# Performance work log

Measured on AMD Instinct MI355X. Metric: run time of the kernel, lower is better.

## Reference

```python
import jax, jax.numpy as jnp
import numpy as np

N = 8192
H_CHANNELS = 2048
HEADS = 16
D = H_CHANNELS // HEADS  # 128


def setup_inputs() -> dict:
    key = jax.random.key(0)
    k1, k2, k3 = jax.random.split(key, 3)
    x0 = jax.random.normal(k1, (N, H_CHANNELS), dtype=jnp.float32)
    # boolean mask: True entries are masked out (set to -inf)
    mask = jax.random.randint(k2, (N, N), 0, 2).astype(jnp.bool_)
    # torch Linear weight layout: [out_features, in_features] = [3*d, h_channels]
    W_qkv = jax.random.normal(k3, (3 * D, H_CHANNELS), dtype=jnp.float32) * (1.0 / np.sqrt(H_CHANNELS))
    return {"x0": x0, "mask": mask, "W_qkv": W_qkv}


def reference(x0, mask, W_qkv):
    # qkv = x0 @ W^T : [N, 3d]
    qkv = x0 @ W_qkv.T
    q, k, v = jnp.split(qkv, 3, axis=-1)          # each [N, d]
    att_logits = (q @ k.T) / D                    # [N, N]  (note: scale is /d, not /sqrt(d))
    att_logits = jnp.where(mask, -jnp.inf, att_logits)
    att = jax.nn.softmax(att_logits, axis=-1)     # [N, N]
    # dropout p=0.0 (eval mode) -> identity
    return att @ v                                # [N, d]
```

## Files before the change

kernel.cpp:

```cpp
#include <hip/hip_runtime.h>
#include <hip/hip_bf16.h>

typedef __attribute__((ext_vector_type(8))) short short8;
typedef __attribute__((ext_vector_type(4))) float f32x4;
typedef __attribute__((ext_vector_type(16))) float f32x16;
typedef __attribute__((ext_vector_type(2))) unsigned int uint2v;

#define NTOK 8192
#define HCH  2048
#define DDIM 128
#define NSPLIT 8
#define KPS   (NTOK / NSPLIT)
#define NITER (KPS / 64)

__device__ __forceinline__ unsigned short f2bf(float f) {
    __hip_bfloat16 h = __float2bfloat16(f);
    return *reinterpret_cast<unsigned short*>(&h);
}
__device__ __forceinline__ unsigned short f2h(float f) {
    _Float16 h = (_Float16)f;
    return *reinterpret_cast<unsigned short*>(&h);
}

__device__ __forceinline__ void gload_lds16(const void* g, void* l) {
    __builtin_amdgcn_global_load_lds(
        reinterpret_cast<const __attribute__((address_space(1))) unsigned int*>(
            reinterpret_cast<uintptr_t>(g)),
        reinterpret_cast<__attribute__((address_space(3))) unsigned int*>(
            reinterpret_cast<uintptr_t>(l)),
        16, 0, 0);
}

__global__ void detect_kernel(const unsigned int* __restrict__ X,
                              const unsigned int* __restrict__ M,
                              int* __restrict__ flags)
{
    const int lane = threadIdx.x & 63;
    unsigned int e = (X[lane] >> 7) & 0xFF;
    unsigned long long hb = __ballot(e >= 110 && e <= 140);

    bool w_ok = true, h_ok = true, b_ok = true;
#pragma unroll
    for (int i = 0; i < 16; i++) {
        unsigned int u = M[lane + 64 * i];
        if (!(u == 0u || u == 1u || u == 0x3F800000u)) w_ok = false;
        unsigned int h0 = u & 0xFFFFu, h1 = u >> 16;
        bool o0 = (h0 == 0u || h0 == 0x3F80u || h0 == 0x3C00u || h0 == 1u);
        bool o1 = (h1 == 0u || h1 == 0x3F80u || h1 == 0x3C00u || h1 == 1u);
        if (!(o0 && o1)) h_ok = false;
        unsigned int b0 = u & 0xFF, b1 = (u >> 8) & 0xFF,
                     b2 = (u >> 16) & 0xFF, b3 = u >> 24;
        if (b0 > 1u || b1 > 1u || b2 > 1u || b3 > 1u) b_ok = false;
    }
    bool allw = __all(w_ok), allh = __all(h_ok), allb = __all(b_ok);
    if (lane == 0) {
        flags[0] = (__popcll(hb) < 32) ? 1 : 0;
        flags[1] = allw ? 0 : (allb ? 1 : (allh ? 2 : 3));
    }
}

__global__ __launch_bounds__(256) void conv_w(
    const void* __restrict__ Wv, const int* __restrict__ flags,
    unsigned short* __restrict__ Wbf)
{
    int t = blockIdx.x * 256 + threadIdx.x;
    size_t off = (size_t)t * 8;
    if (flags[0] != 0) {
        const float* Wf = (const float*)Wv;
        float4 a = *reinterpret_cast<const float4*>(Wf + off);
        float4 b = *reinterpret_cast<const float4*>(Wf + off + 4);
        unsigned short o[8] = { f2bf(a.x), f2bf(a.y), f2bf(a.z), f2bf(a.w),
                                f2bf(b.x), f2bf(b.y), f2bf(b.z), f2bf(b.w) };
        *reinterpret_cast<uint4*>(Wbf + off) = *reinterpret_cast<uint4*>(o);
    } else {
        *reinterpret_cast<uint4*>(Wbf + off) =
            *reinterpret_cast<const uint4*>((const unsigned short*)Wv + off);
    }
}

__global__ __launch_bounds__(256) void conv_x(
    const void* __restrict__ Xv, const int* __restrict__ flags,
    unsigned short* __restrict__ Xbf)
{
    int t = blockIdx.x * 256 + threadIdx.x;
    size_t off = (size_t)t * 8;
    if (flags[0] != 0) {
        const float* Xf = (const float*)Xv;
        float4 a = *reinterpret_cast<const float4*>(Xf + off);
        float4 b = *reinterpret_cast<const float4*>(Xf + off + 4);
        unsigned short o[8] = { f2bf(a.x), f2bf(a.y), f2bf(a.z), f2bf(a.w),
                                f2bf(b.x), f2bf(b.y), f2bf(b.z), f2bf(b.w) };
        *reinterpret_cast<uint4*>(Xbf + off) = *reinterpret_cast<uint4*>(o);
    } else {
        *reinterpret_cast<uint4*>(Xbf + off) =
            *reinterpret_cast<const uint4*>((const unsigned short*)Xv + off);
    }
}

__global__ __launch_bounds__(256) void mask_pack(
    const void* __restrict__ maskv, const int* __restrict__ flags,
    unsigned char* __restrict__ Mp)
{
    const int mmode = flags[1];
    const int NB = NTOK * (NTOK / 8);
    int t0 = blockIdx.x * 256 + threadIdx.x;
    for (int b = t0; b < NB; b += 2048 * 256) {
        unsigned int byte = 0;
        if (mmode == 0) {
            const uint4* p = reinterpret_cast<const uint4*>(
                (const unsigned int*)maskv + (size_t)b * 8);
            uint4 a = p[0], c = p[1];
            byte = (a.x != 0u) | ((a.y != 0u) << 1) | ((a.z != 0u) << 2) | ((a.w != 0u) << 3)
                 | ((c.x != 0u) << 4) | ((c.y != 0u) << 5) | ((c.z != 0u) << 6) | ((c.w != 0u) << 7);
        } else if (mmode == 1) {
            unsigned long long v = *reinterpret_cast<const unsigned long long*>(
                (const unsigned char*)maskv + (size_t)b * 8);
#pragma unroll
            for (int k = 0; k < 8; k++)
                byte |= (((v >> (8 * k)) & 0xFFull) != 0ull) << k;
        } else if (mmode == 2) {
            uint4 a = *reinterpret_cast<const uint4*>(
                (const unsigned short*)maskv + (size_t)b * 8);
            byte = ((a.x & 0xFFFFu) != 0u) | ((a.x >> 16 != 0u) << 1)
                 | (((a.y & 0xFFFFu) != 0u) << 2) | ((a.y >> 16 != 0u) << 3)
                 | (((a.z & 0xFFFFu) != 0u) << 4) | ((a.z >> 16 != 0u) << 5)
                 | (((a.w & 0xFFFFu) != 0u) << 6) | ((a.w >> 16 != 0u) << 7);
        } else {
            byte = ((const unsigned char*)maskv)[b];
        }
        Mp[b] = (unsigned char)byte;
    }
}

__global__ __launch_bounds__(256) void qkv_gemm(
    const unsigned short* __restrict__ Xbf, const unsigned short* __restrict__ Wbf,
    unsigned short* __restrict__ Qb, unsigned short* __restrict__ Kb,
    unsigned short* __restrict__ Vb)
{
    __shared__ unsigned short Wsm[128 * 64];
    __shared__ unsigned short Xsm[32 * 64];
    const int tid  = threadIdx.x;
    const int lane = tid & 63, w = tid >> 6;
    const int c = lane & 15, g = lane >> 4;
    const int q0 = blockIdx.x * 32;
    const int n0 = blockIdx.y * 128;

    f32x4 acc[4];
#pragma unroll
    for (int i = 0; i < 4; i++) acc[i] = (f32x4){0.f, 0.f, 0.f, 0.f};

    const int xrow = tid >> 3, xc8 = tid & 7;
    const int arow = (w & 1) * 16 + c;

    for (int kk = 0; kk < HCH; kk += 64) {
        __syncthreads();
#pragma unroll
        for (int i = 0; i < 4; i++) {
            int cid = tid + 256 * i;
            int n = cid >> 3, c8 = cid & 7;
            gload_lds16(Wbf + (size_t)(n0 + n) * HCH + kk + ((c8 ^ (n & 7)) * 8),
                        &Wsm[cid * 8]);
        }
        gload_lds16(Xbf + (size_t)(q0 + xrow) * HCH + kk + ((xc8 ^ (xrow & 7)) * 8),
                    &Xsm[tid * 8]);
        __syncthreads();
#pragma unroll
        for (int ks = 0; ks < 2; ks++) {
            short8 af = *reinterpret_cast<const short8*>(
                &Xsm[(arow * 8 + ((ks * 4 + g) ^ (c & 7))) * 8]);
#pragma unroll
            for (int nt = 0; nt < 4; nt++) {
                int n = (w >> 1) * 64 + nt * 16 + c;
                short8 bf = *reinterpret_cast<const short8*>(
                    &Wsm[(n * 8 + ((ks * 4 + g) ^ (c & 7))) * 8]);
                acc[nt] = __builtin_amdgcn_mfma_f32_16x16x32_bf16(af, bf, acc[nt], 0, 0, 0);
            }
        }
    }
    unsigned short* dst = (blockIdx.y == 0) ? Qb : (blockIdx.y == 1) ? Kb : Vb;
#pragma unroll
    for (int nt = 0; nt < 4; nt++) {
        int n = (w >> 1) * 64 + nt * 16 + c;
#pragma unroll
        for (int r = 0; r < 4; r++) {
            int rr = q0 + (w & 1) * 16 + g * 4 + r;
            dst[(size_t)rr * DDIM + n] = f2bf(acc[nt][r]);
        }
    }
}

__global__ __launch_bounds__(256) void vtrans(
    const unsigned short* __restrict__ V, unsigned short* __restrict__ VT)
{
    __shared__ unsigned short T[32 * 33];
    const int t = threadIdx.x;
    const int k0 = blockIdx.x * 32, d0 = blockIdx.y * 32;
    {
        int key = t >> 3, dq = (t & 7) * 4;
        ushort4 v = *reinterpret_cast<const ushort4*>(V + (size_t)(k0 + key) * DDIM + d0 + dq);
        T[(dq + 0) * 33 + key] = v.x;
        T[(dq + 1) * 33 + key] = v.y;
        T[(dq + 2) * 33 + key] = v.z;
        T[(dq + 3) * 33 + key] = v.w;
    }
    __syncthreads();
    {
        int d = t >> 3, kq = (t & 7) * 4;
        ushort4 o;
        o.x = T[d * 33 + kq + 0]; o.y = T[d * 33 + kq + 1];
        o.z = T[d * 33 + kq + 2]; o.w = T[d * 33 + kq + 3];
        *reinterpret_cast<ushort4*>(VT + (size_t)(d0 + d) * NTOK + k0 + kq) = o;
    }
}

__global__ __launch_bounds__(256, 1) void attn_part(
    const unsigned short* __restrict__ Qb, const unsigned short* __restrict__ Kb,
    const unsigned short* __restrict__ VT, const unsigned long long* __restrict__ Mp,
    _Float16* __restrict__ Opart, float* __restrict__ lpart)
{
    __shared__ unsigned short Ksm[2][64 * 128];
    __shared__ unsigned short Vsm[2][128 * 64];
    const int tid  = threadIdx.x;
    const int lane = tid & 63, w = tid >> 6;
    const int la = lane & 31, hi = lane >> 5;
    const int split = blockIdx.x;
    const int qb    = blockIdx.y;
    const int q0 = qb * 256;
    const int kbase = split * KPS;
    const int tb0 = kbase >> 6;
    const int qrowA = q0 + w * 64 + la;
    const int qrowB = qrowA + 32;

    auto stage = [&](int b, int tt) {
        const int k0s = kbase + tt * 64;
#pragma unroll
        for (int i = 0; i < 4; i++) {
            int cid = tid + 256 * i;
            int rowk = cid >> 4, c16 = cid & 15;
            gload_lds16(Kb + (size_t)(k0s + rowk) * DDIM + ((c16 ^ (rowk & 15)) * 8),
                        &Ksm[b][cid * 8]);
        }
#pragma unroll
        for (int i = 0; i < 4; i++) {
            int cid = tid + 256 * i;
            int d = cid >> 3, c8 = cid & 7;
            gload_lds16(VT + (size_t)d * NTOK + k0s + ((c8 ^ (d & 7)) * 8),
                        &Vsm[b][cid * 8]);
        }
    };

    short8 qfA[8], qfB[8];
#pragma unroll
    for (int dstep = 0; dstep < 8; dstep++) {
        qfA[dstep] = *reinterpret_cast<const short8*>(
            Qb + (size_t)qrowA * DDIM + dstep * 16 + hi * 8);
        qfB[dstep] = *reinterpret_cast<const short8*>(
            Qb + (size_t)qrowB * DDIM + dstep * 16 + hi * 8);
    }

    f32x16 accO[2][4];
#pragma unroll
    for (int qh = 0; qh < 2; qh++)
#pragma unroll
        for (int dt = 0; dt < 4; dt++)
#pragma unroll
            for (int r = 0; r < 16; r++) accO[qh][dt][r] = 0.f;
    float LaccA = 0.f, LaccB = 0.f;

    unsigned long long mwA = Mp[(size_t)qrowA * 128 + tb0];
    unsigned long long mwB = Mp[(size_t)qrowB * 128 + tb0];
    unsigned long long mwnA = 0, mwnB = 0;

    stage(0, 0);

    for (int t = 0; t < NITER; t++) {
        __syncthreads();
        if (t + 1 < NITER) {
            stage((t + 1) & 1, t + 1);
            mwnA = Mp[(size_t)qrowA * 128 + tb0 + t + 1];
            mwnB = Mp[(size_t)qrowB * 128 + tb0 + t + 1];
        }
        const unsigned short* Ks = Ksm[t & 1];
        const unsigned short* Vs = Vsm[t & 1];

        f32x16 S0A, S1A, S0B, S1B;
#pragma unroll
        for (int r = 0; r < 16; r++) { S0A[r] = 0.f; S1A[r] = 0.f; S0B[r] = 0.f; S1B[r] = 0.f; }
#pragma unroll
        for (int dstep = 0; dstep < 8; dstep++) {
            int slot = (2 * dstep + hi) ^ (la & 15);
            short8 k0f = *reinterpret_cast<const short8*>(&Ks[(la * 16 + slot) * 8]);
            short8 k1f = *reinterpret_cast<const short8*>(&Ks[((32 + la) * 16 + slot) * 8]);
            S0A = __builtin_amdgcn_mfma_f32_32x32x16_bf16(k0f, qfA[dstep], S0A, 0, 0, 0);
            S1A = __builtin_amdgcn_mfma_f32_32x32x16_bf16(k1f, qfA[dstep], S1A, 0, 0, 0);
            S0B = __builtin_amdgcn_mfma_f32_32x32x16_bf16(k0f, qfB[dstep], S0B, 0, 0, 0);
            S1B = __builtin_amdgcn_mfma_f32_32x32x16_bf16(k1f, qfB[dstep], S1B, 0, 0, 0);
        }

        short8 paA[4], paB[4];
        auto softpack = [&](const f32x16& S, int kt, short8* paP,
                            unsigned long long mh, float& Lacc) {
            float p[16];
#pragma unroll
            for (int r = 0; r < 16; r++) {
                int bit = kt * 32 + (r & 3) + 8 * (r >> 2);
                bool mv = (mh >> bit) & 1ull;
                float e = __expf(S[r] * 0.0078125f);
                p[r] = mv ? 0.f : e;
                Lacc += p[r];
            }
            unsigned int U[4][2];
#pragma unroll
            for (int b = 0; b < 4; b++) {
                asm("v_cvt_pk_bf16_f32 %0, %1, %2"
                    : "=v"(U[b][0]) : "v"(p[4 * b + 0]), "v"(p[4 * b + 1]));
                asm("v_cvt_pk_bf16_f32 %0, %1, %2"
                    : "=v"(U[b][1]) : "v"(p[4 * b + 2]), "v"(p[4 * b + 3]));
            }
#pragma unroll
            for (int h = 0; h < 2; h++) {
                uint2v sA = __builtin_amdgcn_permlane32_swap(U[2 * h][0], U[2 * h + 1][0], false, false);
                uint2v sB = __builtin_amdgcn_permlane32_swap(U[2 * h][1], U[2 * h + 1][1], false, false);
                unsigned int fr[4] = { sA.x, sB.x, sA.y, sB.y };
                paP[h] = *reinterpret_cast<short8*>(fr);
            }
        };
        const unsigned long long mhA = mwA >> (4 * hi);
        const unsigned long long mhB = mwB >> (4 * hi);
        softpack(S0A, 0, &paA[0], mhA, LaccA);
        softpack(S1A, 1, &paA[2], mhA, LaccA);
        softpack(S0B, 0, &paB[0], mhB, LaccB);
        softpack(S1B, 1, &paB[2], mhB, LaccB);

#pragma unroll
        for (int s = 0; s < 4; s++) {
#pragma unroll
            for (int dt = 0; dt < 4; dt++) {
                int slot = (2 * s + hi) ^ (la & 7);
                short8 vf = *reinterpret_cast<const short8*>(
                    &Vs[((dt * 32 + la) * 8 + slot) * 8]);
                accO[0][dt] = __builtin_amdgcn_mfma_f32_32x32x16_bf16(paA[s], vf, accO[0][dt], 0, 0, 0);
                accO[1][dt] = __builtin_amdgcn_mfma_f32_32x32x16_bf16(paB[s], vf, accO[1][dt], 0, 0, 0);
            }
        }
        if (t + 1 < NITER) { mwA = mwnA; mwB = mwnB; }
    }

    LaccA += __shfl_xor(LaccA, 32, 64);
    LaccB += __shfl_xor(LaccB, 32, 64);

    _Float16* Ob = Opart + ((size_t)split * 32 + qb) * (256 * DDIM) + (size_t)w * 8192;
#pragma unroll
    for (int qh = 0; qh < 2; qh++)
#pragma unroll
        for (int dt = 0; dt < 4; dt++)
#pragma unroll
            for (int b = 0; b < 4; b++) {
                unsigned int w0 = (unsigned int)f2h(accO[qh][dt][4 * b + 0])
                                | ((unsigned int)f2h(accO[qh][dt][4 * b + 1]) << 16);
                unsigned int w1 = (unsigned int)f2h(accO[qh][dt][4 * b + 2])
                                | ((unsigned int)f2h(accO[qh][dt][4 * b + 3]) << 16);
                uint2 uv; uv.x = w0; uv.y = w1;
                *reinterpret_cast<uint2*>(
                    Ob + (size_t)((((qh * 4 + dt) * 4 + b) * 64 + lane) * 4)) = uv;
            }
    if (hi == 0) {
        lpart[(size_t)split * NTOK + q0 + w * 64 + la] = LaccA;
        lpart[(size_t)split * NTOK + q0 + w * 64 + 32 + la] = LaccB;
    }
}

__global__ __launch_bounds__(256) void combine(
    const _Float16* __restrict__ Opart, const float* __restrict__ lpart,
    float* __restrict__ out)
{
    int cid = blockIdx.x * 256 + threadIdx.x;
    int l  = cid & 63;
    int b  = (cid >> 6) & 3;
    int dt = (cid >> 8) & 3;
    int qh = (cid >> 10) & 1;
    int w  = (cid >> 11) & 3;
    int qb = cid >> 13;
    int la = l & 31, hi = l >> 5;
    int d  = dt * 32 + la;
    int rbase = qb * 256 + w * 64 + qh * 32 + 8 * b + 4 * hi;
    size_t off = (size_t)qb * (256 * DDIM) + (size_t)w * 8192
               + (size_t)((((qh * 4 + dt) * 4 + b) * 64 + l) * 4);
    const size_t S = (size_t)NTOK * DDIM;
    float num[4] = {0.f, 0.f, 0.f, 0.f};
    float den[4] = {0.f, 0.f, 0.f, 0.f};
#pragma unroll
    for (int s = 0; s < NSPLIT; s++) {
        uint2 v = *reinterpret_cast<const uint2*>(Opart + (size_t)s * S + off);
        const _Float16* h = reinterpret_cast<const _Float16*>(&v);
#pragma unroll
        for (int j = 0; j < 4; j++) num[j] += (float)h[j];
#pragma unroll
        for (int j = 0; j < 4; j++) den[j] += lpart[(size_t)s * NTOK + rbase + j];
    }
#pragma unroll
    for (int j = 0; j < 4; j++)
        out[(size_t)(rbase + j) * DDIM + d] = (den[j] > 0.f) ? num[j] / den[j] : 0.f;
}

extern "C" void kernel_launch(void* const* d_in, const int* in_sizes, int n_in,
                              void* d_out, int out_size, void* d_ws, size_t ws_size,
                              hipStream_t stream)
{
    const void* X = d_in[0]; const void* mask = d_in[1]; const void* W = d_in[2];
    {
        const void* x_ = nullptr; const void* m_ = nullptr; const void* w_ = nullptr;
        for (int i = 0; i < n_in; i++) {
            if (in_sizes[i] == 16777216) x_ = d_in[i];
            else if (in_sizes[i] == 67108864) m_ = d_in[i];
            else if (in_sizes[i] == 786432) w_ = d_in[i];
        }
        if (x_ && m_ && w_) { X = x_; mask = m_; W = w_; }
    }
    float* out = (float*)d_out;

    char* ws = (char*)d_ws;
    unsigned short* Qb  = (unsigned short*)(ws);
    unsigned short* Kb  = (unsigned short*)(ws + (2ull << 20));
    unsigned short* VT  = (unsigned short*)(ws + (4ull << 20));
    unsigned long long* Mpk = (unsigned long long*)(ws + (6ull << 20));
    _Float16*       Opart = (_Float16*)(ws + (14ull << 20));
    unsigned short* Wbf = (unsigned short*)(ws + (14ull << 20));
    unsigned short* Vb  = (unsigned short*)(ws + (14ull << 20) + (1536ull << 10));
    float*          lpart = (float*)(ws + (30ull << 20));
    int*            flags = (int*)(ws + (30ull << 20) + (512ull << 10));
    unsigned short* Xbf = (unsigned short*)(ws + (32ull << 20));

    detect_kernel<<<1, 64, 0, stream>>>((const unsigned int*)X, (const unsigned int*)mask, flags);
    conv_w<<<dim3(384), 256, 0, stream>>>(W, flags, Wbf);
    conv_x<<<dim3(8192), 256, 0, stream>>>(X, flags, Xbf);
    mask_pack<<<dim3(2048), 256, 0, stream>>>(mask, flags, (unsigned char*)Mpk);
    qkv_gemm<<<dim3(256, 3), 256, 0, stream>>>(Xbf, Wbf, Qb, Kb, Vb);
    vtrans<<<dim3(256, 4), 256, 0, stream>>>(Vb, VT);
    attn_part<<<dim3(NSPLIT, 32), 256, 0, stream>>>(Qb, Kb, VT, Mpk, Opart, lpart);
    combine<<<dim3(1024), 256, 0, stream>>>(Opart, lpart, out);
}
```

Before: 509.3 us.

## Enlarge QKV GEMM tile with double-buffered LDS and merge conversion kernels

The QKV GEMM block tile grows from 32x128 to 128x128, and each wave now computes a 4x4 grid of MFMA tiles instead of 1x4, so every loaded weight tile is reused across more rows. LDS is double-buffered so the next K-slice is staged while the current one is being computed. The X and W conversion kernels are merged into one launch. The trade-off is far fewer GEMM blocks (192, roughly one wave of blocks on the device), plus more LDS use and more registers per thread.

```diff
diff --git a/kernel.cpp b/kernel.cpp
--- a/kernel.cpp
+++ b/kernel.cpp
@@ -59,41 +59,26 @@
     }
 }
 
-__global__ __launch_bounds__(256) void conv_w(
-    const void* __restrict__ Wv, const int* __restrict__ flags,
-    unsigned short* __restrict__ Wbf)
-{
-    int t = blockIdx.x * 256 + threadIdx.x;
+__global__ __launch_bounds__(256) void conv_xw(
+    const void* __restrict__ Xv, const void* __restrict__ Wv,
+    const int* __restrict__ flags,
+    unsigned short* __restrict__ Xbf, unsigned short* __restrict__ Wbf)
+{
+    const bool isW = (blockIdx.x >= 8192);
+    const void* src = isW ? Wv : Xv;
+    unsigned short* dst = isW ? Wbf : Xbf;
+    int t = (isW ? (blockIdx.x - 8192) : blockIdx.x) * 256 + threadIdx.x;
     size_t off = (size_t)t * 8;
     if (flags[0] != 0) {
-        const float* Wf = (const float*)Wv;
-        float4 a = *reinterpret_cast<const float4*>(Wf + off);
-        float4 b = *reinterpret_cast<const float4*>(Wf + off + 4);
+        const float* Sf = (const float*)src;
+        float4 a = *reinterpret_cast<const float4*>(Sf + off);
+        float4 b = *reinterpret_cast<const float4*>(Sf + off + 4);
         unsigned short o[8] = { f2bf(a.x), f2bf(a.y), f2bf(a.z), f2bf(a.w),
                                 f2bf(b.x), f2bf(b.y), f2bf(b.z), f2bf(b.w) };
-        *reinterpret_cast<uint4*>(Wbf + off) = *reinterpret_cast<uint4*>(o);
+        *reinterpret_cast<uint4*>(dst + off) = *reinterpret_cast<uint4*>(o);
     } else {
-        *reinterpret_cast<uint4*>(Wbf + off) =
-            *reinterpret_cast<const uint4*>((const unsigned short*)Wv + off);
-    }
-}
-
-__global__ __launch_bounds__(256) void conv_x(
-    const void* __restrict__ Xv, const int* __restrict__ flags,
-    unsigned short* __restrict__ Xbf)
-{
-    int t = blockIdx.x * 256 + threadIdx.x;
-    size_t off = (size_t)t * 8;
-    if (flags[0] != 0) {
-        const float* Xf = (const float*)Xv;
-        float4 a = *reinterpret_cast<const float4*>(Xf + off);
-        float4 b = *reinterpret_cast<const float4*>(Xf + off + 4);
-        unsigned short o[8] = { f2bf(a.x), f2bf(a.y), f2bf(a.z), f2bf(a.w),
-                                f2bf(b.x), f2bf(b.y), f2bf(b.z), f2bf(b.w) };
-        *reinterpret_cast<uint4*>(Xbf + off) = *reinterpret_cast<uint4*>(o);
-    } else {
-        *reinterpret_cast<uint4*>(Xbf + off) =
-            *reinterpret_cast<const uint4*>((const unsigned short*)Xv + off);
+        *reinterpret_cast<uint4*>(dst + off) =
+            *reinterpret_cast<const uint4*>((const unsigned short*)src + off);
     }
 }
 
@@ -137,56 +122,79 @@
     unsigned short* __restrict__ Qb, unsigned short* __restrict__ Kb,
     unsigned short* __restrict__ Vb)
 {
-    __shared__ unsigned short Wsm[128 * 64];
-    __shared__ unsigned short Xsm[32 * 64];
+    __shared__ unsigned short Xsm[2][128 * 64];
+    __shared__ unsigned short Wsm[2][128 * 64];
     const int tid  = threadIdx.x;
     const int lane = tid & 63, w = tid >> 6;
     const int c = lane & 15, g = lane >> 4;
-    const int q0 = blockIdx.x * 32;
+    const int q0 = blockIdx.x * 128;
     const int n0 = blockIdx.y * 128;
 
-    f32x4 acc[4];
-#pragma unroll
-    for (int i = 0; i < 4; i++) acc[i] = (f32x4){0.f, 0.f, 0.f, 0.f};
-
-    const int xrow = tid >> 3, xc8 = tid & 7;
-    const int arow = (w & 1) * 16 + c;
-
-    for (int kk = 0; kk < HCH; kk += 64) {
-        __syncthreads();
+    auto stage = [&](int b, int kk) {
 #pragma unroll
         for (int i = 0; i < 4; i++) {
             int cid = tid + 256 * i;
-            int n = cid >> 3, c8 = cid & 7;
-            gload_lds16(Wbf + (size_t)(n0 + n) * HCH + kk + ((c8 ^ (n & 7)) * 8),
-                        &Wsm[cid * 8]);
-        }
-        gload_lds16(Xbf + (size_t)(q0 + xrow) * HCH + kk + ((xc8 ^ (xrow & 7)) * 8),
-                    &Xsm[tid * 8]);
+            int row = cid >> 3, c8 = cid & 7;
+            gload_lds16(Xbf + (size_t)(q0 + row) * HCH + kk + ((c8 ^ (row & 7)) * 8),
+                        &Xsm[b][cid * 8]);
+        }
+#pragma unroll
+        for (int i = 0; i < 4; i++) {
+            int cid = tid + 256 * i;
+            int row = cid >> 3, c8 = cid & 7;
+            gload_lds16(Wbf + (size_t)(n0 + row) * HCH + kk + ((c8 ^ (row & 7)) * 8),
+                        &Wsm[b][cid * 8]);
+        }
+    };
+
+    f32x4 acc[4][4];
+#pragma unroll
+    for (int mt = 0; mt < 4; mt++)
+#pragma unroll
+        for (int nt = 0; nt < 4; nt++) acc[mt][nt] = (f32x4){0.f, 0.f, 0.f, 0.f};
+
+    stage(0, 0);
+
+    const int NKIT = HCH / 64;
+    for (int t = 0; t < NKIT; t++) {
         __syncthreads();
+        if (t + 1 < NKIT) stage((t + 1) & 1, (t + 1) * 64);
+        const unsigned short* Xs = Xsm[t & 1];
+        const unsigned short* Ws = Wsm[t & 1];
 #pragma unroll
         for (int ks = 0; ks < 2; ks++) {
-            short8 af = *reinterpret_cast<const short8*>(
-                &Xsm[(arow * 8 + ((ks * 4 + g) ^ (c & 7))) * 8]);
+            const int slot = (ks * 4 + g) ^ (c & 7);
+            short8 af[4], bf[4];
+#pragma unroll
+            for (int mt = 0; mt < 4; mt++) {
+                int a = (w & 1) * 64 + mt * 16 + c;
+                af[mt] = *reinterpret_cast<const short8*>(&Xs[(a * 8 + slot) * 8]);
+            }
 #pragma unroll
             for (int nt = 0; nt < 4; nt++) {
-                int n = (w >> 1) * 64 + nt * 16 + c;
-                short8 bf = *reinterpret_cast<const short8*>(
-                    &Wsm[(n * 8 + ((ks * 4 + g) ^ (c & 7))) * 8]);
-                acc[nt] = __builtin_amdgcn_mfma_f32_16x16x32_bf16(af, bf, acc[nt], 0, 0, 0);
-            }
+                int b = (w >> 1) * 64 + nt * 16 + c;
+                bf[nt] = *reinterpret_cast<const short8*>(&Ws[(b * 8 + slot) * 8]);
+            }
+#pragma unroll
+            for (int mt = 0; mt < 4; mt++)
+#pragma unroll
+                for (int nt = 0; nt < 4; nt++)
+                    acc[mt][nt] = __builtin_amdgcn_mfma_f32_16x16x32_bf16(
+                        af[mt], bf[nt], acc[mt][nt], 0, 0, 0);
         }
     }
     unsigned short* dst = (blockIdx.y == 0) ? Qb : (blockIdx.y == 1) ? Kb : Vb;
 #pragma unroll
-    for (int nt = 0; nt < 4; nt++) {
-        int n = (w >> 1) * 64 + nt * 16 + c;
-#pragma unroll
-        for (int r = 0; r < 4; r++) {
-            int rr = q0 + (w & 1) * 16 + g * 4 + r;
-            dst[(size_t)rr * DDIM + n] = f2bf(acc[nt][r]);
-        }
-    }
+    for (int mt = 0; mt < 4; mt++)
+#pragma unroll
+        for (int nt = 0; nt < 4; nt++) {
+            int col = (w >> 1) * 64 + nt * 16 + c;
+#pragma unroll
+            for (int r = 0; r < 4; r++) {
+                int rr = q0 + (w & 1) * 64 + mt * 16 + g * 4 + r;
+                dst[(size_t)rr * DDIM + col] = f2bf(acc[mt][nt][r]);
+            }
+        }
 }
 
 __global__ __launch_bounds__(256) void vtrans(
@@ -432,10 +440,9 @@
     unsigned short* Xbf = (unsigned short*)(ws + (32ull << 20));
 
     detect_kernel<<<1, 64, 0, stream>>>((const unsigned int*)X, (const unsigned int*)mask, flags);
-    conv_w<<<dim3(384), 256, 0, stream>>>(W, flags, Wbf);
-    conv_x<<<dim3(8192), 256, 0, stream>>>(X, flags, Xbf);
+    conv_xw<<<dim3(8192 + 384), 256, 0, stream>>>(X, W, flags, Xbf, Wbf);
     mask_pack<<<dim3(2048), 256, 0, stream>>>(mask, flags, (unsigned char*)Mpk);
-    qkv_gemm<<<dim3(256, 3), 256, 0, stream>>>(Xbf, Wbf, Qb, Kb, Vb);
+    qkv_gemm<<<dim3(64, 3), 256, 0, stream>>>(Xbf, Wbf, Qb, Kb, Vb);
     vtrans<<<dim3(256, 4), 256, 0, stream>>>(Vb, VT);
     attn_part<<<dim3(NSPLIT, 32), 256, 0, stream>>>(Qb, Kb, VT, Mpk, Opart, lpart);
     combine<<<dim3(1024), 256, 0, stream>>>(Opart, lpart, out);
```

After: 499.2 us. 1.02x faster.
